# Optimization experiments

Hardware: AMD Instinct MI355X
Metric: run time of the kernel (lower is better)

The kernel has to match this reference:

```python
import jax, jax.numpy as jnp
import numpy as np

TEMP1 = 4.0  # local_temp1 default


def setup_inputs() -> dict:
    key = jax.random.key(0)
    k1, k2 = jax.random.split(key)
    query = jax.random.normal(k1, (256, 768, 96), dtype=jnp.float32)
    context = jax.random.normal(k2, (256, 768, 19, 19), dtype=jnp.float32)
    return {"query": query, "context": context}


def reference(query, context):
    # query: [B, ndf, Q]; context: [B, ndf, ih, iw]
    B, ndf, Q = query.shape
    ih, iw = context.shape[2], context.shape[3]
    S = ih * iw
    ctx = context.reshape(B, ndf, S)            # [B, ndf, S]
    # attn = contextT @ query -> [B, S, Q]
    attn = jnp.einsum('bds,bdq->bsq', ctx, query)
    # softmax over query dim
    attn = jax.nn.softmax(attn, axis=-1)
    # transpose to [B, Q, S], temperature scale, softmax over source dim
    attn = jnp.swapaxes(attn, 1, 2) * TEMP1
    attn = jax.nn.softmax(attn, axis=-1)        # [B, Q, S]
    # weightedContext = context @ attn^T -> [B, ndf, Q]
    weighted_context = jnp.einsum('bds,bqs->bdq', ctx, attn)
    attn_map = attn.reshape(B, Q, ih, iw)
    return weighted_context, attn_map
```

## Files before the change

### kernel.cpp

```cpp
#include <hip/hip_runtime.h>

#define NB 256
#define NDF 768
#define NQ 96
#define NS 361
#define LDT 40
#define LDP 392
#define WSROW 368
#define WS_LOG_BYTES ((size_t)NB * NQ * WSROW * 2)

typedef short bf16x8_t __attribute__((ext_vector_type(8)));
typedef float f32x4_t __attribute__((ext_vector_type(4)));
typedef float f32x4u_t __attribute__((ext_vector_type(4), aligned(4)));
typedef unsigned int u32x4_t __attribute__((ext_vector_type(4)));

__device__ __forceinline__ unsigned pack_hi(unsigned b_, unsigned a_) {
    return __builtin_amdgcn_perm(b_, a_, 0x07060302u);
}
__device__ __forceinline__ unsigned short f2bf(float x) {
    unsigned u = __float_as_uint(x);
    u += 0x7FFFu + ((u >> 16) & 1u);
    return (unsigned short)(u >> 16);
}
__device__ __forceinline__ float bf2f(unsigned short h) {
    return __uint_as_float(((unsigned)h) << 16);
}

__device__ __forceinline__ void cvt8(const float* x, bf16x8_t& hi, bf16x8_t& lo) {
    unsigned uh[8]; float fl[8];
#pragma unroll
    for (int j = 0; j < 8; ++j) {
        unsigned u = __float_as_uint(x[j]);
        uh[j] = u;
        fl[j] = x[j] - __uint_as_float(u & 0xFFFF0000u);
    }
    u32x4_t h, l;
    h[0] = pack_hi(uh[1], uh[0]); h[1] = pack_hi(uh[3], uh[2]);
    h[2] = pack_hi(uh[5], uh[4]); h[3] = pack_hi(uh[7], uh[6]);
    l[0] = pack_hi(__float_as_uint(fl[1]), __float_as_uint(fl[0]));
    l[1] = pack_hi(__float_as_uint(fl[3]), __float_as_uint(fl[2]));
    l[2] = pack_hi(__float_as_uint(fl[5]), __float_as_uint(fl[4]));
    l[3] = pack_hi(__float_as_uint(fl[7]), __float_as_uint(fl[6]));
    hi = __builtin_bit_cast(bf16x8_t, h);
    lo = __builtin_bit_cast(bf16x8_t, l);
}

__device__ __forceinline__ void block_sync_lds() {
    __builtin_amdgcn_sched_barrier(0x20);
    asm volatile("s_waitcnt lgkmcnt(0)" ::: "memory");
    __builtin_amdgcn_sched_barrier(0x20);
    __builtin_amdgcn_s_barrier();
    __builtin_amdgcn_sched_barrier(0x20);
}

template<int MODE>
__global__ __launch_bounds__(384, 3) void k1_gemm1_softmaxq(
    const float* __restrict__ Qg, const float* __restrict__ Cg,
    unsigned short* __restrict__ WsLog, float* __restrict__ AoutF)
{
    __shared__ __align__(16) unsigned short sQhi[2][NQ * LDT];
    __shared__ __align__(16) unsigned short sQlo[2][NQ * LDT];

    const int x = blockIdx.x;
    const int b = (x & 7) * 32 + (x >> 4);
    const int h = (x >> 3) & 1;

    const int tid = threadIdx.x;
    const int wv = tid >> 6;
    const int lane = tid & 63;
    const int ll = lane & 15;
    const int lg = lane >> 4;
    const int s0 = 192 * h;
    const int qq = tid % 96;
    const int koct = tid / 96;
    const int sc0 = min(s0 + 32 * wv + ll, NS - 1);
    const int sc1 = min(s0 + 32 * wv + 16 + ll, NS - 1);

    const float* __restrict__ qg = Qg + (size_t)b * NDF * NQ;
    const float* __restrict__ cg = Cg + (size_t)b * NDF * NS;

    f32x4_t acc[6][2];
#pragma unroll
    for (int i = 0; i < 6; ++i)
#pragma unroll
        for (int j = 0; j < 2; ++j) acc[i][j] = (f32x4_t)0.0f;

    float rq[8];

#define LOADQ(K0) { \
    _Pragma("unroll") \
    for (int j = 0; j < 8; ++j) \
        rq[j] = qg[((K0) + 8 * koct + j) * NQ + qq]; }

#define STAGEQ(BUF) { \
    bf16x8_t qh, ql; \
    cvt8(rq, qh, ql); \
    *(bf16x8_t*)&sQhi[BUF][qq * LDT + 8 * koct] = qh; \
    *(bf16x8_t*)&sQlo[BUF][qq * LDT + 8 * koct] = ql; }

    LOADQ(0);
    STAGEQ(0);
    block_sync_lds();

    for (int k0 = 0; k0 < NDF; k0 += 32) {
        const int cur = (k0 >> 5) & 1;
        float c0v[8], c1v[8];
#pragma unroll
        for (int j = 0; j < 8; ++j) c0v[j] = cg[(size_t)(k0 + 8 * lg + j) * NS + sc0];
#pragma unroll
        for (int j = 0; j < 8; ++j) c1v[j] = cg[(size_t)(k0 + 8 * lg + j) * NS + sc1];
        if (k0 + 32 < NDF) LOADQ(k0 + 32);
        bf16x8_t B0h, B0l, B1h, B1l;
        cvt8(c0v, B0h, B0l);
        cvt8(c1v, B1h, B1l);
#pragma unroll
        for (int mt = 0; mt < 6; ++mt) {
            bf16x8_t Ah = *(const bf16x8_t*)&sQhi[cur][(16 * mt + ll) * LDT + 8 * lg];
            bf16x8_t Al = *(const bf16x8_t*)&sQlo[cur][(16 * mt + ll) * LDT + 8 * lg];
            acc[mt][0] = __builtin_amdgcn_mfma_f32_16x16x32_bf16(Ah, B0h, acc[mt][0], 0, 0, 0);
            acc[mt][0] = __builtin_amdgcn_mfma_f32_16x16x32_bf16(Ah, B0l, acc[mt][0], 0, 0, 0);
            acc[mt][0] = __builtin_amdgcn_mfma_f32_16x16x32_bf16(Al, B0h, acc[mt][0], 0, 0, 0);
            acc[mt][1] = __builtin_amdgcn_mfma_f32_16x16x32_bf16(Ah, B1h, acc[mt][1], 0, 0, 0);
            acc[mt][1] = __builtin_amdgcn_mfma_f32_16x16x32_bf16(Ah, B1l, acc[mt][1], 0, 0, 0);
            acc[mt][1] = __builtin_amdgcn_mfma_f32_16x16x32_bf16(Al, B1h, acc[mt][1], 0, 0, 0);
        }
        if (k0 + 32 < NDF) STAGEQ(cur ^ 1);
        block_sync_lds();
    }
#undef LOADQ
#undef STAGEQ

#pragma unroll
    for (int nt = 0; nt < 2; ++nt) {
        float m = -3.0e38f;
#pragma unroll
        for (int mt = 0; mt < 6; ++mt)
#pragma unroll
            for (int r = 0; r < 4; ++r) m = fmaxf(m, acc[mt][nt][r]);
        m = fmaxf(m, __shfl_xor(m, 16));
        m = fmaxf(m, __shfl_xor(m, 32));
        float sum = 0.0f;
#pragma unroll
        for (int mt = 0; mt < 6; ++mt)
#pragma unroll
            for (int r = 0; r < 4; ++r) {
                float e = __expf(acc[mt][nt][r] - m);
                acc[mt][nt][r] = e;
                sum += e;
            }
        sum += __shfl_xor(sum, 16);
        sum += __shfl_xor(sum, 32);
        float inv = 4.0f / sum;
#pragma unroll
        for (int mt = 0; mt < 6; ++mt)
#pragma unroll
            for (int r = 0; r < 4; ++r) acc[mt][nt][r] *= inv;
    }

    if constexpr (MODE >= 1) {
        unsigned short* wr = WsLog + (size_t)b * NQ * WSROW;
#pragma unroll
        for (int mt = 0; mt < 6; ++mt)
#pragma unroll
            for (int nt = 0; nt < 2; ++nt)
#pragma unroll
                for (int r = 0; r < 4; ++r) {
                    int q = 16 * mt + 4 * lg + r;
                    int s = s0 + 32 * wv + 16 * nt + ll;
                    if (s < NS) wr[q * WSROW + s] = f2bf(acc[mt][nt][r]);
                }
    } else {
        float* aout = AoutF + (size_t)b * NQ * NS;
#pragma unroll
        for (int mt = 0; mt < 6; ++mt)
#pragma unroll
            for (int nt = 0; nt < 2; ++nt)
#pragma unroll
                for (int r = 0; r < 4; ++r) {
                    int q = 16 * mt + 4 * lg + r;
                    int s = s0 + 32 * wv + 16 * nt + ll;
                    if (s < NS) aout[(size_t)q * NS + s] = acc[mt][nt][r];
                }
    }
}

__global__ __launch_bounds__(256) void k15_softmaxs(float* __restrict__ Aout)
{
    const int b = blockIdx.x;
    const int q = blockIdx.y * 4 + (threadIdx.x >> 6);
    const int lane = threadIdx.x & 63;
    float* __restrict__ row = Aout + ((size_t)b * NQ + q) * NS;
    const int c0 = 6 * lane;

    float v[6];
#pragma unroll
    for (int i = 0; i < 6; ++i) v[i] = (c0 + i < NS) ? row[c0 + i] : -INFINITY;
    float m = v[0];
#pragma unroll
    for (int i = 1; i < 6; ++i) m = fmaxf(m, v[i]);
#pragma unroll
    for (int o = 1; o < 64; o <<= 1) m = fmaxf(m, __shfl_xor(m, o));
    float e[6], sum = 0.0f;
#pragma unroll
    for (int i = 0; i < 6; ++i) { e[i] = __expf(v[i] - m); sum += e[i]; }
#pragma unroll
    for (int o = 1; o < 64; o <<= 1) sum += __shfl_xor(sum, o);
    float inv = 1.0f / sum;
#pragma unroll
    for (int i = 0; i < 6; ++i) if (c0 + i < NS) row[c0 + i] = e[i] * inv;
}

template<bool FUSED>
__global__ __launch_bounds__(512, 4) void k2_gemm2(
    const float* __restrict__ Cg, const unsigned short* __restrict__ WsLog,
    const float* __restrict__ AttnF, float* __restrict__ Wout, float* __restrict__ AoutF)
{
    extern __shared__ char smem2[];
    unsigned short* sP = (unsigned short*)smem2;
    unsigned* sPd = (unsigned*)smem2;
    float* sMax = (float*)(smem2 + NQ * LDP * 2);
    float* sInv = sMax + NQ;

    const int x = blockIdx.x;
    const int b = (x & 7) * 32 + (x >> 5);
    const int quarter = (x >> 3) & 3;
    const int tid = threadIdx.x;
    const int wv = tid >> 6;
    const int lane = tid & 63;
    const int ll = lane & 15;
    const int lg = lane >> 4;

    if constexpr (FUSED) {
        const unsigned* __restrict__ wsd = (const unsigned*)(WsLog + (size_t)b * NQ * WSROW);
        for (int i = tid; i < NQ * 184; i += 512) {
            int r = i / 184, c = i - r * 184;
            sPd[r * 196 + c] = wsd[i];
        }
        for (int i = tid; i < NQ * 12; i += 512) {
            int r = i / 12, c = i - r * 12;
            sPd[r * 196 + 184 + c] = 0;
        }
        __syncthreads();

        const int l32 = tid & 31;
        const int rbase = tid >> 5;
#pragma unroll
        for (int pass = 0; pass < 6; ++pass) {
            int row = pass * 16 + rbase;
            float m = -3.0e38f;
#pragma unroll
            for (int j = 0; j < 6; ++j) {
                int dw = l32 + 32 * j;
                if (dw < 184) {
                    unsigned u = sPd[row * 196 + dw];
                    float v0 = bf2f((unsigned short)(u & 0xFFFFu));
                    float v1 = bf2f((unsigned short)(u >> 16));
                    if (2 * dw < NS) m = fmaxf(m, v0);
                    if (2 * dw + 1 < NS) m = fmaxf(m, v1);
                }
            }
#pragma unroll
            for (int o = 1; o < 32; o <<= 1) m = fmaxf(m, __shfl_xor(m, o));
            if (l32 == 0) sMax[row] = m;
        }
        __syncthreads();
#pragma unroll
        for (int pass = 0; pass < 6; ++pass) {
            int row = pass * 16 + rbase;
            float m = sMax[row];
            float sum = 0.0f;
#pragma unroll
            for (int j = 0; j < 6; ++j) {
                int dw = l32 + 32 * j;
                if (dw < 184) {
                    unsigned u = sPd[row * 196 + dw];
                    float v0 = bf2f((unsigned short)(u & 0xFFFFu));
                    float v1 = bf2f((unsigned short)(u >> 16));
                    float e0 = (2 * dw < NS) ? __expf(v0 - m) : 0.0f;
                    float e1 = (2 * dw + 1 < NS) ? __expf(v1 - m) : 0.0f;
                    sum += e0 + e1;
                    sPd[row * 196 + dw] = ((unsigned)f2bf(e1) << 16) | (unsigned)f2bf(e0);
                }
            }
#pragma unroll
            for (int o = 1; o < 32; o <<= 1) sum += __shfl_xor(sum, o);
            if (l32 == 0) sInv[row] = sum;
        }
        __syncthreads();
        if (tid < NQ) sInv[tid] = 1.0f / sInv[tid];
        __syncthreads();
        if (quarter == 0) {
            float* aout = AoutF + (size_t)b * NQ * NS;
            for (int i = tid; i < NQ * NS; i += 512) {
                int q = i / NS, s = i - q * NS;
                aout[i] = bf2f(sP[q * LDP + s]) * sInv[q];
            }
        }
    } else {
        const float* __restrict__ attn = AttnF + (size_t)b * NQ * NS;
        for (int i = tid; i < NQ * 181; i += 512) {
            int row = i / 181, p = i - row * 181;
            float x0 = attn[row * NS + 2 * p];
            float x1 = (p < 180) ? attn[row * NS + 2 * p + 1] : 0.0f;
            sPd[row * 196 + p] = pack_hi(__float_as_uint(x1), __float_as_uint(x0));
        }
        for (int i = tid; i < NQ * 15; i += 512) {
            int row = i / 15, p = i - row * 15;
            sPd[row * 196 + 181 + p] = 0;
        }
        __syncthreads();
    }

    f32x4_t acc[3][3];
#pragma unroll
    for (int i = 0; i < 3; ++i)
#pragma unroll
        for (int j = 0; j < 3; ++j) acc[i][j] = (f32x4_t)0.0f;

    const int dw = wv >> 1, qw = wv & 1;
    const float* __restrict__ cq = Cg + (size_t)b * NDF * NS + (size_t)(quarter * 192) * NS;

#pragma unroll
    for (int c = 0; c < 12; ++c) {
        bf16x8_t Bf[3];
#pragma unroll
        for (int nt = 0; nt < 3; ++nt) {
            int row = 16 * (3 * qw + nt) + ll;
            Bf[nt] = *(const bf16x8_t*)&sP[row * LDP + 32 * c + 8 * lg];
        }
#pragma unroll
        for (int i = 0; i < 3; ++i) {
            int d = 16 * (3 * dw + i) + ll;
            const float* ap = cq + (size_t)d * NS + 32 * c + 8 * lg;
            u32x4_t u;
            if (c < 11) {
                f32x4u_t a0 = *(const f32x4u_t*)ap;
                f32x4u_t a1 = *(const f32x4u_t*)(ap + 4);
                u[0] = pack_hi(__float_as_uint(a0[1]), __float_as_uint(a0[0]));
                u[1] = pack_hi(__float_as_uint(a0[3]), __float_as_uint(a0[2]));
                u[2] = pack_hi(__float_as_uint(a1[1]), __float_as_uint(a1[0]));
                u[3] = pack_hi(__float_as_uint(a1[3]), __float_as_uint(a1[2]));
            } else {
                float t[8];
#pragma unroll
                for (int e = 0; e < 8; ++e) {
                    int s = 352 + 8 * lg + e;
                    t[e] = (s < NS) ? ap[e] : 0.0f;
                }
                u[0] = pack_hi(__float_as_uint(t[1]), __float_as_uint(t[0]));
                u[1] = pack_hi(__float_as_uint(t[3]), __float_as_uint(t[2]));
                u[2] = pack_hi(__float_as_uint(t[5]), __float_as_uint(t[4]));
                u[3] = pack_hi(__float_as_uint(t[7]), __float_as_uint(t[6]));
            }
            bf16x8_t Af = __builtin_bit_cast(bf16x8_t, u);
#pragma unroll
            for (int nt = 0; nt < 3; ++nt)
                acc[i][nt] = __builtin_amdgcn_mfma_f32_16x16x32_bf16(Af, Bf[nt], acc[i][nt], 0, 0, 0);
        }
    }

    float* wout = Wout + (size_t)b * NDF * NQ;
    float invq[3];
#pragma unroll
    for (int nt = 0; nt < 3; ++nt) {
        if constexpr (FUSED) invq[nt] = sInv[16 * (3 * qw + nt) + ll];
        else invq[nt] = 1.0f;
    }
#pragma unroll
    for (int i = 0; i < 3; ++i)
#pragma unroll
        for (int nt = 0; nt < 3; ++nt)
#pragma unroll
            for (int r = 0; r < 4; ++r) {
                int d = quarter * 192 + 16 * (3 * dw + i) + 4 * lg + r;
                int q = 16 * (3 * qw + nt) + ll;
                wout[(size_t)d * NQ + q] = acc[i][nt][r] * invq[nt];
            }
}

extern "C" void kernel_launch(void* const* d_in, const int* in_sizes, int n_in,
                              void* d_out, int out_size, void* d_ws, size_t ws_size,
                              hipStream_t stream) {
    const float* Qg = (const float*)d_in[0];
    const float* Cg = (const float*)d_in[1];
    float* Wout = (float*)d_out;
    float* Aout = Wout + (size_t)NB * NDF * NQ;

    const int smem2 = NQ * LDP * 2 + NQ * 8;

    if (ws_size >= WS_LOG_BYTES) {
        unsigned short* wsLog = (unsigned short*)d_ws;
        k1_gemm1_softmaxq<1><<<dim3(NB * 2), dim3(384), 0, stream>>>(Qg, Cg, wsLog, nullptr);
        (void)hipFuncSetAttribute((const void*)k2_gemm2<true>,
                                  hipFuncAttributeMaxDynamicSharedMemorySize, smem2);
        k2_gemm2<true><<<dim3(NB * 4), dim3(512), smem2, stream>>>(
            Cg, wsLog, nullptr, Wout, Aout);
    } else {
        k1_gemm1_softmaxq<0><<<dim3(NB * 2), dim3(384), 0, stream>>>(Qg, Cg, nullptr, Aout);
        k15_softmaxs<<<dim3(NB, 24), dim3(256), 0, stream>>>(Aout);
        (void)hipFuncSetAttribute((const void*)k2_gemm2<false>,
                                  hipFuncAttributeMaxDynamicSharedMemorySize, smem2);
        k2_gemm2<false><<<dim3(NB * 4), dim3(512), smem2, stream>>>(
            Cg, nullptr, Aout, Wout, Aout);
    }
}
```

Measured before the change: 209.0 us.

## Software-pipeline context loads and double the K-step in GEMM1 kernel

The first GEMM loop now steps 64 along K per iteration, staging two 32-wide query slices into shared memory per barrier. Context values for the next half-step are prefetched into registers (cA/cB ping-pong), and sched_barriers keep the loads issued ahead of the MFMA phases. The aim is to hide global load latency behind matrix work and halve the number of block barriers. The cost is higher register pressure (48 staging floats) and twice the LDS footprint, which may hurt occupancy at 3 blocks per CU.

```diff
diff --git a/kernel.cpp b/kernel.cpp
--- a/kernel.cpp
+++ b/kernel.cpp
@@ -58,8 +58,8 @@
     const float* __restrict__ Qg, const float* __restrict__ Cg,
     unsigned short* __restrict__ WsLog, float* __restrict__ AoutF)
 {
-    __shared__ __align__(16) unsigned short sQhi[2][NQ * LDT];
-    __shared__ __align__(16) unsigned short sQlo[2][NQ * LDT];
+    __shared__ __align__(16) unsigned short sQhi[2][2][NQ * LDT];
+    __shared__ __align__(16) unsigned short sQlo[2][2][NQ * LDT];
 
     const int x = blockIdx.x;
     const int b = (x & 7) * 32 + (x >> 4);
@@ -85,50 +85,67 @@
 #pragma unroll
         for (int j = 0; j < 2; ++j) acc[i][j] = (f32x4_t)0.0f;
 
-    float rq[8];
-
-#define LOADQ(K0) { \
+    float cA[16], cB[16], qv[16];
+
+#define LOADQ64(K0) { \
+    _Pragma("unroll") \
+    for (int t = 0; t < 2; ++t) \
+        _Pragma("unroll") \
+        for (int j = 0; j < 8; ++j) \
+            qv[8 * t + j] = qg[((K0) + 32 * t + 8 * koct + j) * NQ + qq]; }
+
+#define STAGEQ64(BUF) { \
+    bf16x8_t h0, l0, h1, l1; \
+    cvt8(qv, h0, l0); cvt8(qv + 8, h1, l1); \
+    *(bf16x8_t*)&sQhi[BUF][0][qq * LDT + 8 * koct] = h0; \
+    *(bf16x8_t*)&sQlo[BUF][0][qq * LDT + 8 * koct] = l0; \
+    *(bf16x8_t*)&sQhi[BUF][1][qq * LDT + 8 * koct] = h1; \
+    *(bf16x8_t*)&sQlo[BUF][1][qq * LDT + 8 * koct] = l1; }
+
+#define LOADCTX(K0, R) { \
     _Pragma("unroll") \
     for (int j = 0; j < 8; ++j) \
-        rq[j] = qg[((K0) + 8 * koct + j) * NQ + qq]; }
-
-#define STAGEQ(BUF) { \
-    bf16x8_t qh, ql; \
-    cvt8(rq, qh, ql); \
-    *(bf16x8_t*)&sQhi[BUF][qq * LDT + 8 * koct] = qh; \
-    *(bf16x8_t*)&sQlo[BUF][qq * LDT + 8 * koct] = ql; }
-
-    LOADQ(0);
-    STAGEQ(0);
+        R[j] = cg[(size_t)((K0) + 8 * lg + j) * NS + sc0]; \
+    _Pragma("unroll") \
+    for (int j = 0; j < 8; ++j) \
+        R[8 + j] = cg[(size_t)((K0) + 8 * lg + j) * NS + sc1]; }
+
+#define MFMAPHASE(R, BUF, HALF) { \
+    bf16x8_t B0h, B0l, B1h, B1l; \
+    cvt8(R, B0h, B0l); \
+    cvt8(R + 8, B1h, B1l); \
+    _Pragma("unroll") \
+    for (int mt = 0; mt < 6; ++mt) { \
+        bf16x8_t Ah = *(const bf16x8_t*)&sQhi[BUF][HALF][(16 * mt + ll) * LDT + 8 * lg]; \
+        bf16x8_t Al = *(const bf16x8_t*)&sQlo[BUF][HALF][(16 * mt + ll) * LDT + 8 * lg]; \
+        acc[mt][0] = __builtin_amdgcn_mfma_f32_16x16x32_bf16(Ah, B0h, acc[mt][0], 0, 0, 0); \
+        acc[mt][0] = __builtin_amdgcn_mfma_f32_16x16x32_bf16(Ah, B0l, acc[mt][0], 0, 0, 0); \
+        acc[mt][0] = __builtin_amdgcn_mfma_f32_16x16x32_bf16(Al, B0h, acc[mt][0], 0, 0, 0); \
+        acc[mt][1] = __builtin_amdgcn_mfma_f32_16x16x32_bf16(Ah, B1h, acc[mt][1], 0, 0, 0); \
+        acc[mt][1] = __builtin_amdgcn_mfma_f32_16x16x32_bf16(Ah, B1l, acc[mt][1], 0, 0, 0); \
+        acc[mt][1] = __builtin_amdgcn_mfma_f32_16x16x32_bf16(Al, B1h, acc[mt][1], 0, 0, 0); } }
+
+    LOADQ64(0);
+    LOADCTX(0, cA);
+    STAGEQ64(0);
     block_sync_lds();
 
-    for (int k0 = 0; k0 < NDF; k0 += 32) {
-        const int cur = (k0 >> 5) & 1;
-        float c0v[8], c1v[8];
-#pragma unroll
-        for (int j = 0; j < 8; ++j) c0v[j] = cg[(size_t)(k0 + 8 * lg + j) * NS + sc0];
-#pragma unroll
-        for (int j = 0; j < 8; ++j) c1v[j] = cg[(size_t)(k0 + 8 * lg + j) * NS + sc1];
-        if (k0 + 32 < NDF) LOADQ(k0 + 32);
-        bf16x8_t B0h, B0l, B1h, B1l;
-        cvt8(c0v, B0h, B0l);
-        cvt8(c1v, B1h, B1l);
-#pragma unroll
-        for (int mt = 0; mt < 6; ++mt) {
-            bf16x8_t Ah = *(const bf16x8_t*)&sQhi[cur][(16 * mt + ll) * LDT + 8 * lg];
-            bf16x8_t Al = *(const bf16x8_t*)&sQlo[cur][(16 * mt + ll) * LDT + 8 * lg];
-            acc[mt][0] = __builtin_amdgcn_mfma_f32_16x16x32_bf16(Ah, B0h, acc[mt][0], 0, 0, 0);
-            acc[mt][0] = __builtin_amdgcn_mfma_f32_16x16x32_bf16(Ah, B0l, acc[mt][0], 0, 0, 0);
-            acc[mt][0] = __builtin_amdgcn_mfma_f32_16x16x32_bf16(Al, B0h, acc[mt][0], 0, 0, 0);
-            acc[mt][1] = __builtin_amdgcn_mfma_f32_16x16x32_bf16(Ah, B1h, acc[mt][1], 0, 0, 0);
-            acc[mt][1] = __builtin_amdgcn_mfma_f32_16x16x32_bf16(Ah, B1l, acc[mt][1], 0, 0, 0);
-            acc[mt][1] = __builtin_amdgcn_mfma_f32_16x16x32_bf16(Al, B1h, acc[mt][1], 0, 0, 0);
-        }
-        if (k0 + 32 < NDF) STAGEQ(cur ^ 1);
+    for (int k0 = 0; k0 < NDF; k0 += 64) {
+        const int cur = (k0 >> 6) & 1;
+        LOADCTX(k0 + 32, cB);
+        if (k0 + 64 < NDF) LOADQ64(k0 + 64);
+        __builtin_amdgcn_sched_barrier(0);
+        MFMAPHASE(cA, cur, 0);
+        if (k0 + 64 < NDF) LOADCTX(k0 + 64, cA);
+        __builtin_amdgcn_sched_barrier(0);
+        MFMAPHASE(cB, cur, 1);
+        if (k0 + 64 < NDF) STAGEQ64(cur ^ 1);
         block_sync_lds();
     }
-#undef LOADQ
-#undef STAGEQ
+#undef LOADQ64
+#undef STAGEQ64
+#undef LOADCTX
+#undef MFMAPHASE
 
 #pragma unroll
     for (int nt = 0; nt < 2; ++nt) {
```

After: 354.3 us. 1.7x slower.

## Software-pipeline GEMM1 global loads with inline asm and swizzle LDS Q tiles

Applied to the files above, without the earlier changes.

Restructures the GEMM1 k-loop into a hand-pipelined double-register scheme. Context and query loads for the next 32-wide k chunk are issued with inline-asm global_load_dword before the MFMAs on the current chunk run, and explicit vmcnt waits gate each use. The Q LDS tile also gets an XOR swizzle on its 8-element columns to cut bank conflicts on the reads and writes. The aim is to hide global memory latency behind MFMA work, at the cost of more live registers under the 384x3 launch bound and fragile hand-counted vmcnt values.

```diff
diff --git a/kernel.cpp b/kernel.cpp
--- a/kernel.cpp
+++ b/kernel.cpp
@@ -46,12 +46,14 @@
 }
 
 __device__ __forceinline__ void block_sync_lds() {
-    __builtin_amdgcn_sched_barrier(0x20);
     asm volatile("s_waitcnt lgkmcnt(0)" ::: "memory");
-    __builtin_amdgcn_sched_barrier(0x20);
     __builtin_amdgcn_s_barrier();
-    __builtin_amdgcn_sched_barrier(0x20);
-}
+    __builtin_amdgcn_sched_barrier(0);
+}
+
+#define GLD(D, A)     asm volatile("global_load_dword %0, %1, off" : "=v"(D) : "v"(A))
+#define GLDO(D, A, O) asm volatile("global_load_dword %0, %1, off offset:" #O : "=v"(D) : "v"(A))
+#define VMWAIT(N) { asm volatile("s_waitcnt vmcnt(" #N ")"); __builtin_amdgcn_sched_barrier(0); }
 
 template<int MODE>
 __global__ __launch_bounds__(384, 3) void k1_gemm1_softmaxq(
@@ -70,11 +72,13 @@
     const int lane = tid & 63;
     const int ll = lane & 15;
     const int lg = lane >> 4;
+    const int llh = (ll >> 3) & 1;
     const int s0 = 192 * h;
     const int qq = tid % 96;
     const int koct = tid / 96;
     const int sc0 = min(s0 + 32 * wv + ll, NS - 1);
     const int sc1 = min(s0 + 32 * wv + 16 + ll, NS - 1);
+    const int stoff = qq * LDT + 8 * (koct ^ ((qq >> 3) & 3));
 
     const float* __restrict__ qg = Qg + (size_t)b * NDF * NQ;
     const float* __restrict__ cg = Cg + (size_t)b * NDF * NS;
@@ -85,50 +89,79 @@
 #pragma unroll
         for (int j = 0; j < 2; ++j) acc[i][j] = (f32x4_t)0.0f;
 
-    float rq[8];
-
-#define LOADQ(K0) { \
+    float qv[8], cA[16], cB[16];
+
+#define ISSUE_Q(K0) { \
+    unsigned long long qa = (unsigned long long)(qg + ((K0) + 8 * koct) * NQ + qq); \
+    GLD (qv[0], qa);        GLDO(qv[1], qa, 384); \
+    GLDO(qv[2], qa, 768);   GLDO(qv[3], qa, 1152); \
+    GLDO(qv[4], qa, 1536);  GLDO(qv[5], qa, 1920); \
+    GLDO(qv[6], qa, 2304);  GLDO(qv[7], qa, 2688); }
+
+#define ISSUE_CTX(K0, R) { \
+    unsigned long long p0 = (unsigned long long)(cg + (size_t)((K0) + 8 * lg) * NS + sc0); \
+    unsigned long long p1 = p0 + 3u * NS * 4u; \
+    unsigned long long p2 = p0 + 6u * NS * 4u; \
+    GLD (R[0], p0); GLDO(R[1], p0, 1444); GLDO(R[2], p0, 2888); \
+    GLD (R[3], p1); GLDO(R[4], p1, 1444); GLDO(R[5], p1, 2888); \
+    GLD (R[6], p2); GLDO(R[7], p2, 1444); \
+    unsigned long long p3 = (unsigned long long)(cg + (size_t)((K0) + 8 * lg) * NS + sc1); \
+    unsigned long long p4 = p3 + 3u * NS * 4u; \
+    unsigned long long p5 = p3 + 6u * NS * 4u; \
+    GLD (R[8],  p3); GLDO(R[9],  p3, 1444); GLDO(R[10], p3, 2888); \
+    GLD (R[11], p4); GLDO(R[12], p4, 1444); GLDO(R[13], p4, 2888); \
+    GLD (R[14], p5); GLDO(R[15], p5, 1444); }
+
+#define STAGEQ(CUR) { \
+    bf16x8_t qh, ql; \
+    cvt8(qv, qh, ql); \
+    *(bf16x8_t*)&sQhi[CUR][stoff] = qh; \
+    *(bf16x8_t*)&sQlo[CUR][stoff] = ql; }
+
+#define MFMAPH(R, CUR) { \
+    bf16x8_t B0h, B0l, B1h, B1l; \
+    cvt8(R, B0h, B0l); \
+    cvt8(R + 8, B1h, B1l); \
     _Pragma("unroll") \
-    for (int j = 0; j < 8; ++j) \
-        rq[j] = qg[((K0) + 8 * koct + j) * NQ + qq]; }
-
-#define STAGEQ(BUF) { \
-    bf16x8_t qh, ql; \
-    cvt8(rq, qh, ql); \
-    *(bf16x8_t*)&sQhi[BUF][qq * LDT + 8 * koct] = qh; \
-    *(bf16x8_t*)&sQlo[BUF][qq * LDT + 8 * koct] = ql; }
-
-    LOADQ(0);
+    for (int mt = 0; mt < 6; ++mt) { \
+        int ro = (16 * mt + ll) * LDT + 8 * (lg ^ ((2 * mt + llh) & 3)); \
+        bf16x8_t Ah = *(const bf16x8_t*)&sQhi[CUR][ro]; \
+        bf16x8_t Al = *(const bf16x8_t*)&sQlo[CUR][ro]; \
+        acc[mt][0] = __builtin_amdgcn_mfma_f32_16x16x32_bf16(Ah, B0h, acc[mt][0], 0, 0, 0); \
+        acc[mt][0] = __builtin_amdgcn_mfma_f32_16x16x32_bf16(Ah, B0l, acc[mt][0], 0, 0, 0); \
+        acc[mt][0] = __builtin_amdgcn_mfma_f32_16x16x32_bf16(Al, B0h, acc[mt][0], 0, 0, 0); \
+        acc[mt][1] = __builtin_amdgcn_mfma_f32_16x16x32_bf16(Ah, B1h, acc[mt][1], 0, 0, 0); \
+        acc[mt][1] = __builtin_amdgcn_mfma_f32_16x16x32_bf16(Ah, B1l, acc[mt][1], 0, 0, 0); \
+        acc[mt][1] = __builtin_amdgcn_mfma_f32_16x16x32_bf16(Al, B1h, acc[mt][1], 0, 0, 0); } }
+
+#define ITER(C, USE, FILL, CUR, NXT) { \
+    ISSUE_Q(((C) + 1) * 32); \
+    ISSUE_CTX(((C) + 1) * 32, FILL); \
+    VMWAIT(24); \
+    MFMAPH(USE, CUR); \
+    VMWAIT(16); \
+    STAGEQ(NXT); \
+    block_sync_lds(); }
+
+    ISSUE_Q(0);
+    ISSUE_CTX(0, cA);
+    VMWAIT(16);
     STAGEQ(0);
     block_sync_lds();
 
-    for (int k0 = 0; k0 < NDF; k0 += 32) {
-        const int cur = (k0 >> 5) & 1;
-        float c0v[8], c1v[8];
-#pragma unroll
-        for (int j = 0; j < 8; ++j) c0v[j] = cg[(size_t)(k0 + 8 * lg + j) * NS + sc0];
-#pragma unroll
-        for (int j = 0; j < 8; ++j) c1v[j] = cg[(size_t)(k0 + 8 * lg + j) * NS + sc1];
-        if (k0 + 32 < NDF) LOADQ(k0 + 32);
-        bf16x8_t B0h, B0l, B1h, B1l;
-        cvt8(c0v, B0h, B0l);
-        cvt8(c1v, B1h, B1l);
-#pragma unroll
-        for (int mt = 0; mt < 6; ++mt) {
-            bf16x8_t Ah = *(const bf16x8_t*)&sQhi[cur][(16 * mt + ll) * LDT + 8 * lg];
-            bf16x8_t Al = *(const bf16x8_t*)&sQlo[cur][(16 * mt + ll) * LDT + 8 * lg];
-            acc[mt][0] = __builtin_amdgcn_mfma_f32_16x16x32_bf16(Ah, B0h, acc[mt][0], 0, 0, 0);
-            acc[mt][0] = __builtin_amdgcn_mfma_f32_16x16x32_bf16(Ah, B0l, acc[mt][0], 0, 0, 0);
-            acc[mt][0] = __builtin_amdgcn_mfma_f32_16x16x32_bf16(Al, B0h, acc[mt][0], 0, 0, 0);
-            acc[mt][1] = __builtin_amdgcn_mfma_f32_16x16x32_bf16(Ah, B1h, acc[mt][1], 0, 0, 0);
-            acc[mt][1] = __builtin_amdgcn_mfma_f32_16x16x32_bf16(Ah, B1l, acc[mt][1], 0, 0, 0);
-            acc[mt][1] = __builtin_amdgcn_mfma_f32_16x16x32_bf16(Al, B1h, acc[mt][1], 0, 0, 0);
-        }
-        if (k0 + 32 < NDF) STAGEQ(cur ^ 1);
-        block_sync_lds();
-    }
-#undef LOADQ
+    for (int c = 0; c < 22; c += 2) {
+        ITER(c,     cA, cB, 0, 1);
+        ITER(c + 1, cB, cA, 1, 0);
+    }
+    ITER(22, cA, cB, 0, 1);
+    VMWAIT(0);
+    MFMAPH(cB, 1);
+
+#undef ISSUE_Q
+#undef ISSUE_CTX
 #undef STAGEQ
+#undef MFMAPH
+#undef ITER
 
 #pragma unroll
     for (int nt = 0; nt < 2; ++nt) {
```

Measured after the change: 206.8 us (median of 2 runs). No clear change (-1.1%).

## Stage context tiles through swizzled LDS using dwordx4 loads in GEMM1

Applied to the files above, without the earlier changes.

The first GEMM kernel now loads both context and query tiles with 16-byte global_load_dwordx4 along the contiguous spatial and query dimensions, instead of strided scalar loads. It splits them into bf16 hi/lo halves and writes them into XOR-swizzled LDS buffers, from which the MFMA fragments are read. Loads for the next chunk are issued before the current chunk's MFMAs. The cost is a single LDS buffer with two barriers per step and scalar 2-byte LDS stores, plus a clamp-and-replicate workaround for the unaligned tail at position 360.

```diff
diff --git a/kernel.cpp b/kernel.cpp
--- a/kernel.cpp
+++ b/kernel.cpp
@@ -26,40 +26,24 @@
     return __uint_as_float(((unsigned)h) << 16);
 }
 
-__device__ __forceinline__ void cvt8(const float* x, bf16x8_t& hi, bf16x8_t& lo) {
-    unsigned uh[8]; float fl[8];
-#pragma unroll
-    for (int j = 0; j < 8; ++j) {
-        unsigned u = __float_as_uint(x[j]);
-        uh[j] = u;
-        fl[j] = x[j] - __uint_as_float(u & 0xFFFF0000u);
-    }
-    u32x4_t h, l;
-    h[0] = pack_hi(uh[1], uh[0]); h[1] = pack_hi(uh[3], uh[2]);
-    h[2] = pack_hi(uh[5], uh[4]); h[3] = pack_hi(uh[7], uh[6]);
-    l[0] = pack_hi(__float_as_uint(fl[1]), __float_as_uint(fl[0]));
-    l[1] = pack_hi(__float_as_uint(fl[3]), __float_as_uint(fl[2]));
-    l[2] = pack_hi(__float_as_uint(fl[5]), __float_as_uint(fl[4]));
-    l[3] = pack_hi(__float_as_uint(fl[7]), __float_as_uint(fl[6]));
-    hi = __builtin_bit_cast(bf16x8_t, h);
-    lo = __builtin_bit_cast(bf16x8_t, l);
-}
-
 __device__ __forceinline__ void block_sync_lds() {
-    __builtin_amdgcn_sched_barrier(0x20);
     asm volatile("s_waitcnt lgkmcnt(0)" ::: "memory");
-    __builtin_amdgcn_sched_barrier(0x20);
     __builtin_amdgcn_s_barrier();
-    __builtin_amdgcn_sched_barrier(0x20);
-}
+    __builtin_amdgcn_sched_barrier(0);
+}
+
+#define GLD4(D, A) asm volatile("global_load_dwordx4 %0, %1, off" : "=v"(D) : "v"(A))
+#define VMWAIT0()  { asm volatile("s_waitcnt vmcnt(0)"); __builtin_amdgcn_sched_barrier(0); }
 
 template<int MODE>
 __global__ __launch_bounds__(384, 3) void k1_gemm1_softmaxq(
     const float* __restrict__ Qg, const float* __restrict__ Cg,
     unsigned short* __restrict__ WsLog, float* __restrict__ AoutF)
 {
-    __shared__ __align__(16) unsigned short sQhi[2][NQ * LDT];
-    __shared__ __align__(16) unsigned short sQlo[2][NQ * LDT];
+    __shared__ __align__(16) unsigned short sShi[192 * LDT];
+    __shared__ __align__(16) unsigned short sSlo[192 * LDT];
+    __shared__ __align__(16) unsigned short sQhi[NQ * LDT];
+    __shared__ __align__(16) unsigned short sQlo[NQ * LDT];
 
     const int x = blockIdx.x;
     const int b = (x & 7) * 32 + (x >> 4);
@@ -71,10 +55,25 @@
     const int ll = lane & 15;
     const int lg = lane >> 4;
     const int s0 = 192 * h;
-    const int qq = tid % 96;
-    const int koct = tid / 96;
-    const int sc0 = min(s0 + 32 * wv + ll, NS - 1);
-    const int sc1 = min(s0 + 32 * wv + 16 + ll, NS - 1);
+
+    int kkC[4], srow[4], scl[4];
+    bool qfix[4];
+#pragma unroll
+    for (int j = 0; j < 4; ++j) {
+        int idx = tid + 384 * j;
+        kkC[j] = idx / 48;
+        srow[j] = (idx % 48) * 4;
+        int sAbs = s0 + srow[j];
+        scl[j] = min(sAbs, NS - 4);
+        qfix[j] = (sAbs >= NS - 1);
+    }
+    int kkQ[2], qrow[2];
+#pragma unroll
+    for (int j = 0; j < 2; ++j) {
+        int idx = tid + 384 * j;
+        kkQ[j] = idx / 24;
+        qrow[j] = (idx % 24) * 4;
+    }
 
     const float* __restrict__ qg = Qg + (size_t)b * NDF * NQ;
     const float* __restrict__ cg = Cg + (size_t)b * NDF * NS;
@@ -85,50 +84,80 @@
 #pragma unroll
         for (int j = 0; j < 2; ++j) acc[i][j] = (f32x4_t)0.0f;
 
-    float rq[8];
-
-#define LOADQ(K0) { \
+    f32x4_t cR0, cR1, cR2, cR3, qR0, qR1;
+
+#define ISSUE(C) { \
+    GLD4(cR0, (unsigned long long)(cg + (size_t)((C) * 32 + kkC[0]) * NS + scl[0])); \
+    GLD4(cR1, (unsigned long long)(cg + (size_t)((C) * 32 + kkC[1]) * NS + scl[1])); \
+    GLD4(cR2, (unsigned long long)(cg + (size_t)((C) * 32 + kkC[2]) * NS + scl[2])); \
+    GLD4(cR3, (unsigned long long)(cg + (size_t)((C) * 32 + kkC[3]) * NS + scl[3])); \
+    GLD4(qR0, (unsigned long long)(qg + (size_t)((C) * 32 + kkQ[0]) * NQ + qrow[0])); \
+    GLD4(qR1, (unsigned long long)(qg + (size_t)((C) * 32 + kkQ[1]) * NQ + qrow[1])); }
+
+#define WR4(R, ROWB, COL, DH, DL, FIXQ) { \
+    int cg_ = (COL) >> 3, co_ = (COL) & 7; \
     _Pragma("unroll") \
-    for (int j = 0; j < 8; ++j) \
-        rq[j] = qg[((K0) + 8 * koct + j) * NQ + qq]; }
-
-#define STAGEQ(BUF) { \
-    bf16x8_t qh, ql; \
-    cvt8(rq, qh, ql); \
-    *(bf16x8_t*)&sQhi[BUF][qq * LDT + 8 * koct] = qh; \
-    *(bf16x8_t*)&sQlo[BUF][qq * LDT + 8 * koct] = ql; }
-
-    LOADQ(0);
-    STAGEQ(0);
+    for (int e = 0; e < 4; ++e) { \
+        int row = (ROWB) + e; \
+        float v_ = (FIXQ) ? R[3] : R[e]; \
+        unsigned u = __float_as_uint(v_); \
+        unsigned short hi_ = (unsigned short)(u >> 16); \
+        float lf = v_ - bf2f(hi_); \
+        unsigned short lo_ = (unsigned short)(__float_as_uint(lf) >> 16); \
+        int cs = ((cg_ ^ ((row >> 3) & 3)) << 3) + co_; \
+        (DH)[row * LDT + cs] = hi_; \
+        (DL)[row * LDT + cs] = lo_; } }
+
+#define CVTWRITE() { \
+    VMWAIT0(); \
+    WR4(cR0, srow[0], kkC[0], sShi, sSlo, qfix[0]); \
+    WR4(cR1, srow[1], kkC[1], sShi, sSlo, qfix[1]); \
+    WR4(cR2, srow[2], kkC[2], sShi, sSlo, qfix[2]); \
+    WR4(cR3, srow[3], kkC[3], sShi, sSlo, qfix[3]); \
+    WR4(qR0, qrow[0], kkQ[0], sQhi, sQlo, false); \
+    WR4(qR1, qrow[1], kkQ[1], sQhi, sQlo, false); }
+
+#define MFMAPH() { \
+    bf16x8_t Bh[2], Bl[2]; \
+    _Pragma("unroll") \
+    for (int nt = 0; nt < 2; ++nt) { \
+        int row = 32 * wv + 16 * nt + ll; \
+        int off = row * LDT + 8 * (lg ^ ((row >> 3) & 3)); \
+        Bh[nt] = *(const bf16x8_t*)&sShi[off]; \
+        Bl[nt] = *(const bf16x8_t*)&sSlo[off]; } \
+    _Pragma("unroll") \
+    for (int mt = 0; mt < 6; ++mt) { \
+        int row = 16 * mt + ll; \
+        int off = row * LDT + 8 * (lg ^ ((row >> 3) & 3)); \
+        bf16x8_t Ah = *(const bf16x8_t*)&sQhi[off]; \
+        bf16x8_t Al = *(const bf16x8_t*)&sQlo[off]; \
+        acc[mt][0] = __builtin_amdgcn_mfma_f32_16x16x32_bf16(Ah, Bh[0], acc[mt][0], 0, 0, 0); \
+        acc[mt][0] = __builtin_amdgcn_mfma_f32_16x16x32_bf16(Ah, Bl[0], acc[mt][0], 0, 0, 0); \
+        acc[mt][0] = __builtin_amdgcn_mfma_f32_16x16x32_bf16(Al, Bh[0], acc[mt][0], 0, 0, 0); \
+        acc[mt][1] = __builtin_amdgcn_mfma_f32_16x16x32_bf16(Ah, Bh[1], acc[mt][1], 0, 0, 0); \
+        acc[mt][1] = __builtin_amdgcn_mfma_f32_16x16x32_bf16(Ah, Bl[1], acc[mt][1], 0, 0, 0); \
+        acc[mt][1] = __builtin_amdgcn_mfma_f32_16x16x32_bf16(Al, Bh[1], acc[mt][1], 0, 0, 0); } }
+
+    ISSUE(0);
+    CVTWRITE();
     block_sync_lds();
 
-    for (int k0 = 0; k0 < NDF; k0 += 32) {
-        const int cur = (k0 >> 5) & 1;
-        float c0v[8], c1v[8];
-#pragma unroll
-        for (int j = 0; j < 8; ++j) c0v[j] = cg[(size_t)(k0 + 8 * lg + j) * NS + sc0];
-#pragma unroll
-        for (int j = 0; j < 8; ++j) c1v[j] = cg[(size_t)(k0 + 8 * lg + j) * NS + sc1];
-        if (k0 + 32 < NDF) LOADQ(k0 + 32);
-        bf16x8_t B0h, B0l, B1h, B1l;
-        cvt8(c0v, B0h, B0l);
-        cvt8(c1v, B1h, B1l);
-#pragma unroll
-        for (int mt = 0; mt < 6; ++mt) {
-            bf16x8_t Ah = *(const bf16x8_t*)&sQhi[cur][(16 * mt + ll) * LDT + 8 * lg];
-            bf16x8_t Al = *(const bf16x8_t*)&sQlo[cur][(16 * mt + ll) * LDT + 8 * lg];
-            acc[mt][0] = __builtin_amdgcn_mfma_f32_16x16x32_bf16(Ah, B0h, acc[mt][0], 0, 0, 0);
-            acc[mt][0] = __builtin_amdgcn_mfma_f32_16x16x32_bf16(Ah, B0l, acc[mt][0], 0, 0, 0);
-            acc[mt][0] = __builtin_amdgcn_mfma_f32_16x16x32_bf16(Al, B0h, acc[mt][0], 0, 0, 0);
-            acc[mt][1] = __builtin_amdgcn_mfma_f32_16x16x32_bf16(Ah, B1h, acc[mt][1], 0, 0, 0);
-            acc[mt][1] = __builtin_amdgcn_mfma_f32_16x16x32_bf16(Ah, B1l, acc[mt][1], 0, 0, 0);
-            acc[mt][1] = __builtin_amdgcn_mfma_f32_16x16x32_bf16(Al, B1h, acc[mt][1], 0, 0, 0);
-        }
-        if (k0 + 32 < NDF) STAGEQ(cur ^ 1);
+#pragma unroll 1
+    for (int c = 0; c < 24; ++c) {
+        if (c < 23) ISSUE(c + 1);
+        __builtin_amdgcn_sched_barrier(0);
+        MFMAPH();
         block_sync_lds();
-    }
-#undef LOADQ
-#undef STAGEQ
+        if (c < 23) {
+            CVTWRITE();
+            block_sync_lds();
+        }
+    }
+
+#undef ISSUE
+#undef WR4
+#undef CVTWRITE
+#undef MFMAPH
 
 #pragma unroll
     for (int nt = 0; nt < 2; ++nt) {
```

Measured after the change: 232.5 us. 1.11x slower.
